# Kernel optimization log

Hardware: AMD Instinct MI355X
Metric: run time of the kernel (lower is better)

The kernel has to match this reference:

```python
import jax, jax.numpy as jnp
import numpy as np

KEY_DIM = 32
NUM_HEADS = 4
B, T, F, D = 32, 64, 128, 64


def _proj_in(x, w, b):
    # x: [B,T,F,D], w: [D,H,K], b: [H,K] -> [B,T,F,H,K]
    return jnp.einsum("btfd,dhk->btfhk", x, w) + b


def _axial_mha(x, wq, bq, wk, bk, wv, bv, wo, bo, axis):
    # Keras MultiHeadAttention with attention_axes=(axis,); dropout inactive at inference.
    scale = 1.0 / np.sqrt(KEY_DIM)
    q = _proj_in(x, wq, bq) * scale
    k = _proj_in(x, wk, bk)
    v = _proj_in(x, wv, bv)
    if axis == 1:  # temporal attention, feature axis acts as batch
        scores = jnp.einsum("bqfhk,bsfhk->bfhqs", q, k)  # [B,F,H,Tq,Tk]
        probs = jax.nn.softmax(scores, axis=-1)
        o = jnp.einsum("bfhqs,bsfhk->bqfhk", probs, v)
    else:  # feature attention, temporal axis acts as batch
        scores = jnp.einsum("btqhk,btshk->bthqs", q, k)  # [B,T,H,Fq,Fk]
        probs = jax.nn.softmax(scores, axis=-1)
        o = jnp.einsum("bthqs,btshk->btqhk", probs, v)
    return jnp.einsum("btfhk,hkd->btfd", o, wo) + bo


def setup_inputs() -> dict:
    key = jax.random.key(0)
    ks = jax.random.split(key, 10)
    std = 0.02
    w = lambda k, shape: (jax.random.normal(k, shape, jnp.float32) * std)
    inp = {"x": jax.random.normal(ks[0], (B, T, F, D), jnp.float32)}
    for i, n in enumerate(["tq", "tk", "tv", "fq", "fk", "fv"]):
        inp[n + "_w"] = w(ks[1 + i], (D, NUM_HEADS, KEY_DIM))
        inp[n + "_b"] = jnp.zeros((NUM_HEADS, KEY_DIM), jnp.float32)
    inp["to_w"] = w(ks[7], (NUM_HEADS, KEY_DIM, D))
    inp["to_b"] = jnp.zeros((D,), jnp.float32)
    inp["fo_w"] = w(ks[8], (NUM_HEADS, KEY_DIM, D))
    inp["fo_b"] = jnp.zeros((D,), jnp.float32)
    return inp


def reference(x, tq_w, tq_b, tk_w, tk_b, tv_w, tv_b, to_w, to_b,
              fq_w, fq_b, fk_w, fk_b, fv_w, fv_b, fo_w, fo_b):
    temporal_out = _axial_mha(x, tq_w, tq_b, tk_w, tk_b, tv_w, tv_b, to_w, to_b, axis=1)
    feature_out = _axial_mha(x, fq_w, fq_b, fk_w, fk_b, fv_w, fv_b, fo_w, fo_b, axis=2)
    return temporal_out + feature_out
```

## Files before the change

kernel.cpp:

```cpp
#include <hip/hip_runtime.h>

typedef unsigned short u16;
typedef unsigned int   u32;
typedef short v8s __attribute__((ext_vector_type(8)));
typedef float v4f __attribute__((ext_vector_type(4)));

#define DEV __device__ __forceinline__
#define MFMA(a,b,c) __builtin_amdgcn_mfma_f32_16x16x32_bf16((a),(b),(c),0,0,0)

constexpr int Bb = 32, Tt = 64, Ff = 128, Dd = 64, Hh = 4, Kk = 32;

DEV u16 f2b(float f) {
    u32 u = __float_as_uint(f);
    return (u16)((u + 0x7fffu + ((u >> 16) & 1u)) >> 16);
}
DEV u32 pk2(float a, float b) {
    u32 r;
    asm("v_cvt_pk_bf16_f32 %0, %1, %2" : "=v"(r) : "v"(a), "v"(b));
    return r;
}

__global__ __launch_bounds__(256)
void prep_weights(const float* __restrict__ tq, const float* __restrict__ tk,
                  const float* __restrict__ tv, const float* __restrict__ fq,
                  const float* __restrict__ fk, const float* __restrict__ fv,
                  const float* __restrict__ to_, const float* __restrict__ fo,
                  u16* __restrict__ ws)
{
    int idx = blockIdx.x * 256 + threadIdx.x;
    if (idx < 49152) {
        int p = idx >> 13, rem = idx & 8191;
        int h = rem >> 11, ch = (rem >> 6) & 31, d = rem & 63;
        const float* w = (p==0)?tq:(p==1)?tk:(p==2)?tv:(p==3)?fq:(p==4)?fk:fv;
        ws[idx] = f2b(w[d*128 + h*32 + ch]);
    } else {
        int i2 = idx - 49152;
        int path = i2 >> 13, rem = i2 & 8191;
        int h = rem >> 11, d = (rem >> 5) & 63, k2 = rem & 31;
        const float* w = path ? fo : to_;
        ws[idx] = f2b(w[h*2048 + k2*64 + d]);
    }
}

template<int NR, int MODE>
__global__ __launch_bounds__(NR*4)
void axial_mfma(const float* __restrict__ x, const u16* __restrict__ wsw,
                const float* __restrict__ bq, const float* __restrict__ bk,
                const float* __restrict__ bv, const float* __restrict__ bo,
                float* __restrict__ out)
{
    constexpr int W   = NR / 16;
    constexpr int QP  = 40;
    constexpr int NRp = NR + 8;
    constexpr int PP  = 40;
    constexpr int o_q  = 0;
    constexpr int o_k  = o_q + NR * QP;
    constexpr int o_vt = o_k + NR * QP;
    constexpr int o_p  = o_vt + 32 * NRp;
    constexpr int SMEM = o_p + NR * PP;
    __shared__ alignas(16) u16 sm[SMEM];

    const int tid  = threadIdx.x;
    const int w    = tid >> 6;
    const int lane = tid & 63;
    const int quad = lane >> 4;
    const int l15  = lane & 15;
    const int bid  = blockIdx.x;

    int base, rstride;
    if (MODE == 0) { int b = bid >> 7, f = bid & 127; base = b*(Tt*Ff*Dd) + f*Dd; rstride = Ff*Dd; }
    else           { base = bid * (Ff*Dd); rstride = Dd; }

    constexpr int PB = (MODE == 0) ? 0 : 3;
    const u16* wql = wsw + (PB+0)*8192;
    const u16* wkl = wsw + (PB+1)*8192;
    const u16* wvl = wsw + (PB+2)*8192;
    const u16* wol = wsw + 49152 + MODE*8192;

    v8s xfrag[2];
#pragma unroll
    for (int ks = 0; ks < 2; ++ks) {
        const float* xp = x + base + (w*16 + l15)*rstride + ks*32 + quad*8;
        float4 a = *reinterpret_cast<const float4*>(xp);
        float4 b = *reinterpret_cast<const float4*>(xp + 4);
        v8s f;
        u32* fu = reinterpret_cast<u32*>(&f);
        fu[0] = pk2(a.x, a.y); fu[1] = pk2(a.z, a.w);
        fu[2] = pk2(b.x, b.y); fu[3] = pk2(b.z, b.w);
        xfrag[ks] = f;
    }

    v4f outAcc[4];
#pragma unroll
    for (int i = 0; i < 4; ++i) outAcc[i] = (v4f){0.f,0.f,0.f,0.f};

    const float scale = 0.17677669529663687f;
    const v4f vzero = (v4f){0.f,0.f,0.f,0.f};
    const int qrow_base = o_q + (w*16+l15)*QP;
    const int prow_base = o_p + (w*16+l15)*PP;

#pragma unroll 1
    for (int h = 0; h < Hh; ++h) {
        __syncthreads();

        {
            const u16* wb = wql + h*2048;
#pragma unroll
            for (int nt = 0; nt < 2; ++nt) {
                v4f acc = vzero;
#pragma unroll
                for (int ks = 0; ks < 2; ++ks) {
                    v8s wf = *reinterpret_cast<const v8s*>(wb + (nt*16+l15)*64 + ks*32 + quad*8);
                    acc = MFMA(wf, xfrag[ks], acc);
                }
                float4 b4 = *reinterpret_cast<const float4*>(bq + h*32 + nt*16 + quad*4);
                u32 lo = pk2((acc[0]+b4.x)*scale, (acc[1]+b4.y)*scale);
                u32 hi = pk2((acc[2]+b4.z)*scale, (acc[3]+b4.w)*scale);
                *reinterpret_cast<uint2*>(&sm[qrow_base + nt*16 + quad*4]) = make_uint2(lo, hi);
            }
        }
        {
            const u16* wb = wkl + h*2048;
#pragma unroll
            for (int nt = 0; nt < 2; ++nt) {
                v4f acc = vzero;
#pragma unroll
                for (int ks = 0; ks < 2; ++ks) {
                    v8s wf = *reinterpret_cast<const v8s*>(wb + (nt*16+l15)*64 + ks*32 + quad*8);
                    acc = MFMA(wf, xfrag[ks], acc);
                }
                float4 b4 = *reinterpret_cast<const float4*>(bk + h*32 + nt*16 + quad*4);
                u32 lo = pk2(acc[0]+b4.x, acc[1]+b4.y);
                u32 hi = pk2(acc[2]+b4.z, acc[3]+b4.w);
                *reinterpret_cast<uint2*>(&sm[o_k + (w*16+l15)*QP + nt*16 + quad*4]) = make_uint2(lo, hi);
            }
        }
        {
            const u16* wb = wvl + h*2048;
#pragma unroll
            for (int nt = 0; nt < 2; ++nt) {
                v4f acc = vzero;
#pragma unroll
                for (int ks = 0; ks < 2; ++ks) {
                    v8s wf = *reinterpret_cast<const v8s*>(wb + (nt*16+l15)*64 + ks*32 + quad*8);
                    acc = MFMA(xfrag[ks], wf, acc);
                }
                float bias = bv[h*32 + nt*16 + l15];
                u32 lo = pk2(acc[0]+bias, acc[1]+bias);
                u32 hi = pk2(acc[2]+bias, acc[3]+bias);
                int ch = nt*16 + l15;
                *reinterpret_cast<uint2*>(&sm[o_vt + ch*NRp + w*16 + quad*4]) = make_uint2(lo, hi);
            }
        }
        __syncthreads();

        v8s qf = *reinterpret_cast<const v8s*>(&sm[qrow_base + quad*8]);
        v4f S[W];
#pragma unroll
        for (int ct = 0; ct < W; ++ct) {
            v8s kf = *reinterpret_cast<const v8s*>(&sm[o_k + (ct*16+l15)*QP + quad*8]);
            S[ct] = MFMA(kf, qf, vzero);
        }
        float cm[W];
#pragma unroll
        for (int ct = 0; ct < W; ++ct)
            cm[ct] = fmaxf(fmaxf(S[ct][0], S[ct][1]), fmaxf(S[ct][2], S[ct][3]));
        float mm = cm[0];
#pragma unroll
        for (int ct = 1; ct < W; ++ct) mm = fmaxf(mm, cm[ct]);
        mm = fmaxf(mm, __shfl_xor(mm, 16));
        mm = fmaxf(mm, __shfl_xor(mm, 32));
        float ss = 0.f;
#pragma unroll
        for (int ct = 0; ct < W; ++ct)
#pragma unroll
            for (int r = 0; r < 4; ++r) { float p = __expf(S[ct][r] - mm); S[ct][r] = p; ss += p; }
        ss += __shfl_xor(ss, 16);
        ss += __shfl_xor(ss, 32);
        float rl = 1.f / ss;

        v4f Oacc[2] = { vzero, vzero };
#pragma unroll
        for (int ks = 0; ks < NR/32; ++ks) {
            u32 a0 = pk2(S[2*ks  ][0], S[2*ks  ][1]);
            u32 a1 = pk2(S[2*ks  ][2], S[2*ks  ][3]);
            u32 a2 = pk2(S[2*ks+1][0], S[2*ks+1][1]);
            u32 a3 = pk2(S[2*ks+1][2], S[2*ks+1][3]);
            *reinterpret_cast<uint2*>(&sm[prow_base +      quad*4]) = make_uint2(a0, a1);
            *reinterpret_cast<uint2*>(&sm[prow_base + 16 + quad*4]) = make_uint2(a2, a3);
            v8s pf = *reinterpret_cast<const v8s*>(&sm[prow_base + quad*8]);
#pragma unroll
            for (int nt = 0; nt < 2; ++nt) {
                v8s vf = *reinterpret_cast<const v8s*>(&sm[o_vt + (nt*16+l15)*NRp + ks*32 + quad*8]);
                Oacc[nt] = MFMA(vf, pf, Oacc[nt]);
            }
        }
#pragma unroll
        for (int nt = 0; nt < 2; ++nt) {
            u32 lo = pk2(Oacc[nt][0]*rl, Oacc[nt][1]*rl);
            u32 hi = pk2(Oacc[nt][2]*rl, Oacc[nt][3]*rl);
            *reinterpret_cast<uint2*>(&sm[qrow_base + nt*16 + quad*4]) = make_uint2(lo, hi);
        }

        v8s of = *reinterpret_cast<const v8s*>(&sm[qrow_base + quad*8]);
        {
            const u16* wb = wol + h*2048;
#pragma unroll
            for (int nt = 0; nt < 4; ++nt) {
                v8s wf = *reinterpret_cast<const v8s*>(wb + (nt*16+l15)*32 + quad*8);
                outAcc[nt] = MFMA(wf, of, outAcc[nt]);
            }
        }
    }

    float* orow = out + base + (w*16 + l15)*rstride;
#pragma unroll
    for (int nt = 0; nt < 4; ++nt) {
        int d0 = nt*16 + quad*4;
        float4 b4 = *reinterpret_cast<const float4*>(bo + d0);
        float4 v = make_float4(outAcc[nt][0]+b4.x, outAcc[nt][1]+b4.y,
                               outAcc[nt][2]+b4.z, outAcc[nt][3]+b4.w);
        if (MODE == 1) {
            float4 p = *reinterpret_cast<const float4*>(orow + d0);
            v.x += p.x; v.y += p.y; v.z += p.z; v.w += p.w;
        }
        *reinterpret_cast<float4*>(orow + d0) = v;
    }
}

extern "C" void kernel_launch(void* const* d_in, const int* in_sizes, int n_in,
                              void* d_out, int out_size, void* d_ws, size_t ws_size,
                              hipStream_t stream) {
    const float* x   = (const float*)d_in[0];
    const float* tqw = (const float*)d_in[1];  const float* tqb = (const float*)d_in[2];
    const float* tkw = (const float*)d_in[3];  const float* tkb = (const float*)d_in[4];
    const float* tvw = (const float*)d_in[5];  const float* tvb = (const float*)d_in[6];
    const float* fqw = (const float*)d_in[7];  const float* fqb = (const float*)d_in[8];
    const float* fkw = (const float*)d_in[9];  const float* fkb = (const float*)d_in[10];
    const float* fvw = (const float*)d_in[11]; const float* fvb = (const float*)d_in[12];
    const float* tow = (const float*)d_in[13]; const float* tob = (const float*)d_in[14];
    const float* fow = (const float*)d_in[15]; const float* fob = (const float*)d_in[16];
    float* out = (float*)d_out;
    u16* ws = (u16*)d_ws;

    hipLaunchKernelGGL(prep_weights, dim3(256), dim3(256), 0, stream,
                       tqw, tkw, tvw, fqw, fkw, fvw, tow, fow, ws);
    hipLaunchKernelGGL((axial_mfma<64,0>), dim3(Bb*Ff), dim3(256), 0, stream,
                       x, ws, tqb, tkb, tvb, tob, out);
    hipLaunchKernelGGL((axial_mfma<128,1>), dim3(Bb*Tt), dim3(512), 0, stream,
                       x, ws, fqb, fkb, fvb, fob, out);
}
```

Baseline: 394.2 us.

## Replace LDS round-trips with cross-lane shuffles and double-buffer K/V to drop a barrier

Q, P and O fragments were previously written to shared memory and read back in MFMA operand layout. They are now redistributed across lanes with __shfl inside registers. K and V^T buffers alternate between two shared-memory halves by head parity, so the barrier at the top of each head loop is removed. This is meant to cut LDS traffic and barrier stalls. In exchange it adds many shuffle instructions (ds_bpermute) and more register pressure.

```diff
diff --git a/kernel.cpp b/kernel.cpp
--- a/kernel.cpp
+++ b/kernel.cpp
@@ -4,6 +4,7 @@
 typedef unsigned int   u32;
 typedef short v8s __attribute__((ext_vector_type(8)));
 typedef float v4f __attribute__((ext_vector_type(4)));
+typedef u32   v4u __attribute__((ext_vector_type(4)));
 
 #define DEV __device__ __forceinline__
 #define MFMA(a,b,c) __builtin_amdgcn_mfma_f32_16x16x32_bf16((a),(b),(c),0,0,0)
@@ -18,6 +19,20 @@
     u32 r;
     asm("v_cvt_pk_bf16_f32 %0, %1, %2" : "=v"(r) : "v"(a), "v"(b));
     return r;
+}
+
+DEV v8s redist(u32 lo0, u32 hi0, u32 lo1, u32 hi1, int sA, int sB, int hiHalf) {
+    int aL0 = __shfl((int)lo0, sA), aH0 = __shfl((int)hi0, sA);
+    int aL1 = __shfl((int)lo1, sA), aH1 = __shfl((int)hi1, sA);
+    int bL0 = __shfl((int)lo0, sB), bH0 = __shfl((int)hi0, sB);
+    int bL1 = __shfl((int)lo1, sB), bH1 = __shfl((int)hi1, sB);
+    v4u r;
+    r[0] = (u32)(hiHalf ? aL1 : aL0);
+    r[1] = (u32)(hiHalf ? aH1 : aH0);
+    r[2] = (u32)(hiHalf ? bL1 : bL0);
+    r[3] = (u32)(hiHalf ? bH1 : bH0);
+    union { v4u u; v8s s; } c; c.u = r;
+    return c.s;
 }
 
 __global__ __launch_bounds__(256)
@@ -52,12 +67,8 @@
     constexpr int W   = NR / 16;
     constexpr int QP  = 40;
     constexpr int NRp = NR + 8;
-    constexpr int PP  = 40;
-    constexpr int o_q  = 0;
-    constexpr int o_k  = o_q + NR * QP;
-    constexpr int o_vt = o_k + NR * QP;
-    constexpr int o_p  = o_vt + 32 * NRp;
-    constexpr int SMEM = o_p + NR * PP;
+    constexpr int BUF = NR * QP + 32 * NRp;
+    constexpr int SMEM = 2 * BUF;
     __shared__ alignas(16) u16 sm[SMEM];
 
     const int tid  = threadIdx.x;
@@ -66,6 +77,10 @@
     const int quad = lane >> 4;
     const int l15  = lane & 15;
     const int bid  = blockIdx.x;
+
+    const int sA = ((quad & 1) << 5) | l15;
+    const int sB = sA + 16;
+    const int hiH = quad >> 1;
 
     int base, rstride;
     if (MODE == 0) { int b = bid >> 7, f = bid & 127; base = b*(Tt*Ff*Dd) + f*Dd; rstride = Ff*Dd; }
@@ -96,13 +111,14 @@
 
     const float scale = 0.17677669529663687f;
     const v4f vzero = (v4f){0.f,0.f,0.f,0.f};
-    const int qrow_base = o_q + (w*16+l15)*QP;
-    const int prow_base = o_p + (w*16+l15)*PP;
 
 #pragma unroll 1
     for (int h = 0; h < Hh; ++h) {
-        __syncthreads();
-
+        const int bb   = (h & 1) * BUF;
+        const int o_k  = bb;
+        const int o_vt = bb + NR * QP;
+
+        u32 qlo[2], qhi[2];
         {
             const u16* wb = wql + h*2048;
 #pragma unroll
@@ -114,11 +130,12 @@
                     acc = MFMA(wf, xfrag[ks], acc);
                 }
                 float4 b4 = *reinterpret_cast<const float4*>(bq + h*32 + nt*16 + quad*4);
-                u32 lo = pk2((acc[0]+b4.x)*scale, (acc[1]+b4.y)*scale);
-                u32 hi = pk2((acc[2]+b4.z)*scale, (acc[3]+b4.w)*scale);
-                *reinterpret_cast<uint2*>(&sm[qrow_base + nt*16 + quad*4]) = make_uint2(lo, hi);
-            }
-        }
+                qlo[nt] = pk2((acc[0]+b4.x)*scale, (acc[1]+b4.y)*scale);
+                qhi[nt] = pk2((acc[2]+b4.z)*scale, (acc[3]+b4.w)*scale);
+            }
+        }
+        v8s qf = redist(qlo[0], qhi[0], qlo[1], qhi[1], sA, sB, hiH);
+
         {
             const u16* wb = wkl + h*2048;
 #pragma unroll
@@ -154,7 +171,6 @@
         }
         __syncthreads();
 
-        v8s qf = *reinterpret_cast<const v8s*>(&sm[qrow_base + quad*8]);
         v4f S[W];
 #pragma unroll
         for (int ct = 0; ct < W; ++ct) {
@@ -171,10 +187,15 @@
         mm = fmaxf(mm, __shfl_xor(mm, 16));
         mm = fmaxf(mm, __shfl_xor(mm, 32));
         float ss = 0.f;
-#pragma unroll
-        for (int ct = 0; ct < W; ++ct)
-#pragma unroll
-            for (int r = 0; r < 4; ++r) { float p = __expf(S[ct][r] - mm); S[ct][r] = p; ss += p; }
+        u32 pl[2*W];
+#pragma unroll
+        for (int ct = 0; ct < W; ++ct) {
+            float p0 = __expf(S[ct][0] - mm), p1 = __expf(S[ct][1] - mm);
+            float p2 = __expf(S[ct][2] - mm), p3 = __expf(S[ct][3] - mm);
+            ss += (p0 + p1) + (p2 + p3);
+            pl[2*ct  ] = pk2(p0, p1);
+            pl[2*ct+1] = pk2(p2, p3);
+        }
         ss += __shfl_xor(ss, 16);
         ss += __shfl_xor(ss, 32);
         float rl = 1.f / ss;
@@ -182,27 +203,21 @@
         v4f Oacc[2] = { vzero, vzero };
 #pragma unroll
         for (int ks = 0; ks < NR/32; ++ks) {
-            u32 a0 = pk2(S[2*ks  ][0], S[2*ks  ][1]);
-            u32 a1 = pk2(S[2*ks  ][2], S[2*ks  ][3]);
-            u32 a2 = pk2(S[2*ks+1][0], S[2*ks+1][1]);
-            u32 a3 = pk2(S[2*ks+1][2], S[2*ks+1][3]);
-            *reinterpret_cast<uint2*>(&sm[prow_base +      quad*4]) = make_uint2(a0, a1);
-            *reinterpret_cast<uint2*>(&sm[prow_base + 16 + quad*4]) = make_uint2(a2, a3);
-            v8s pf = *reinterpret_cast<const v8s*>(&sm[prow_base + quad*8]);
+            v8s pf = redist(pl[4*ks], pl[4*ks+1], pl[4*ks+2], pl[4*ks+3], sA, sB, hiH);
 #pragma unroll
             for (int nt = 0; nt < 2; ++nt) {
                 v8s vf = *reinterpret_cast<const v8s*>(&sm[o_vt + (nt*16+l15)*NRp + ks*32 + quad*8]);
                 Oacc[nt] = MFMA(vf, pf, Oacc[nt]);
             }
         }
+        u32 olo[2], ohi[2];
 #pragma unroll
         for (int nt = 0; nt < 2; ++nt) {
-            u32 lo = pk2(Oacc[nt][0]*rl, Oacc[nt][1]*rl);
-            u32 hi = pk2(Oacc[nt][2]*rl, Oacc[nt][3]*rl);
-            *reinterpret_cast<uint2*>(&sm[qrow_base + nt*16 + quad*4]) = make_uint2(lo, hi);
-        }
-
-        v8s of = *reinterpret_cast<const v8s*>(&sm[qrow_base + quad*8]);
+            olo[nt] = pk2(Oacc[nt][0]*rl, Oacc[nt][1]*rl);
+            ohi[nt] = pk2(Oacc[nt][2]*rl, Oacc[nt][3]*rl);
+        }
+        v8s of = redist(olo[0], ohi[0], olo[1], ohi[1], sA, sB, hiH);
+
         {
             const u16* wb = wol + h*2048;
 #pragma unroll
```

After: 384.4 us. -2.5%, faster.
